# Kernel optimization log

Hardware: AMD Instinct MI355X
Metric: run time of the kernel (lower is better)

Reference implementation:

```python
import jax, jax.numpy as jnp
import numpy as np

INITIAL_RADIUS = 1.0  # init_kwargs: initial_radius > 0 -> distance-softmax branch


def reference(xyz, sparse_xyz, sparse_flow, resol_factor, K):
    # xyz: [B,3,N], sparse_xyz: [B,3,M], sparse_flow: [B,3,M]
    q = jnp.transpose(xyz, (0, 2, 1))            # [B,N,3]
    p = jnp.transpose(sparse_xyz, (0, 2, 1))     # [B,M,3]
    flow = jnp.transpose(sparse_flow, (0, 2, 1))  # [B,M,3]

    sigma = INITIAL_RADIUS * resol_factor
    qs = q / sigma
    ps = p / sigma

    # pairwise Euclidean distances [B,N,M]
    sq = (jnp.sum(qs * qs, -1)[:, :, None]
          + jnp.sum(ps * ps, -1)[:, None, :]
          - 2.0 * jnp.einsum('bnc,bmc->bnm', qs, ps))
    dist = jnp.sqrt(jnp.maximum(sq, 1e-12))

    # K nearest: smallest distances
    neg_d, idx = jax.lax.top_k(-dist, K)          # [B,N,K]
    K_dist = -neg_d                               # [B,N,K]

    # gather flow of the K neighbors: [B,N,K,3]
    grouped_flow = jnp.take_along_axis(flow[:, None, :, :], idx[..., None], axis=2)

    # softmax over -distance along K, weighted sum
    K_w = jax.nn.softmax(-K_dist, axis=2)         # [B,N,K]
    dense_flow = jnp.sum(K_w[..., None] * grouped_flow, axis=2)  # [B,N,3]

    return jnp.transpose(dense_flow, (0, 2, 1))   # [B,3,N]


def setup_inputs() -> dict:
    key = jax.random.key(0)
    k1, k2, k3 = jax.random.split(key, 3)
    B, N, M = 4, 16384, 4096
    return {
        'xyz': jax.random.normal(k1, (B, 3, N), dtype=jnp.float32),
        'sparse_xyz': jax.random.normal(k2, (B, 3, M), dtype=jnp.float32),
        'sparse_flow': jax.random.normal(k3, (B, 3, M), dtype=jnp.float32),
        'resol_factor': 1,
        'K': 5,
    }
```

## Files before the change

### kernel.cpp

```cpp
#include <hip/hip_runtime.h>
#include <math.h>
#include <stdint.h>


#define KNN 5
#define GRID 8
#define NCELL (GRID * GRID * GRID)
#define SPAN_TH 64
#define SLICES 8
#define BLOCK (SLICES * 64)
#define EPSM 1e-3f

typedef unsigned int u32;

__device__ __forceinline__ float get_inv_sigma(const int* __restrict__ rf) {
    const int ri = rf[0];
    const float sigma = (ri >= 1 && ri <= 1000000) ? (float)ri : __int_as_float(ri);
    return 1.0f / sigma;
}

__device__ __forceinline__ float rfl_f(float v) {
    return __int_as_float(__builtin_amdgcn_readfirstlane(__float_as_int(v)));
}

__device__ __forceinline__ int cid1(float x, float lo, float ich) {
    const int c = (int)floorf((x - lo) * ich);
    return c < 0 ? 0 : (c > GRID - 1 ? GRID - 1 : c);
}

__device__ __forceinline__ int sp3(int v) {
    return (v & 1) | ((v & 2) << 2) | ((v & 4) << 4);
}

#define CE_FULL(k, ki, c, ci)                          \
    {                                                  \
        const bool sw = (c) < (k);                     \
        const float vmn = fminf(k, c);                 \
        const float vmx = fmaxf(k, c);                 \
        const u32 nki = sw ? (ci) : (ki);              \
        const u32 nci = sw ? (ki) : (ci);              \
        (k) = vmn; (c) = vmx; (ki) = nki; (ci) = nci;  \
    }
#define CE_LAST(k, ki, c, ci)                          \
    {                                                  \
        const bool sw = (c) < (k);                     \
        (ki) = sw ? (ci) : (ki);                       \
        (k) = fminf(k, c);                             \
    }

#define LAD(P, CI)                                     \
    {                                                  \
        float t_ = qx * (P).x;                         \
        t_ = fmaf(qy, (P).y, t_);                      \
        t_ = fmaf(qz, (P).z, t_);                      \
        float c_ = fmaf(-2.0f, t_, (P).w);             \
        u32 ci_ = (u32)(CI);                           \
        CE_FULL(e0, i0, c_, ci_)                       \
        CE_FULL(e1, i1, c_, ci_)                       \
        CE_FULL(e2, i2, c_, ci_)                       \
        CE_FULL(e3, i3, c_, ci_)                       \
        CE_LAST(e4, i4, c_, ci_)                       \
    }


__global__ __launch_bounds__(256)
void prep_kernel(const float* __restrict__ sxyz, const int* __restrict__ rf,
                 float4* __restrict__ pts, int M, int total) {
    const int t = blockIdx.x * 256 + threadIdx.x;
    if (t >= total) return;
    const float inv = get_inv_sigma(rf);
    const int b = t / M, m = t - b * M;
    const float* sb = sxyz + (size_t)b * 3 * M;
    const float x = sb[m] * inv;
    const float y = sb[M + m] * inv;
    const float z = sb[2 * M + m] * inv;
    pts[t] = make_float4(x, y, z, fmaf(x, x, fmaf(y, y, z * z)));
}

template <bool USE_PTS>
__global__ __launch_bounds__(BLOCK, 8)
void knn_kernel(const float* __restrict__ xyz,
                const float* __restrict__ sxyz,
                const float* __restrict__ sflow,
                const int* __restrict__ rf,
                const float4* __restrict__ pts,
                float* __restrict__ out,
                int N, int M) {
    __shared__ float sval_d[SLICES * KNN * 64];
    __shared__ u32   sval_i[SLICES * KNN * 64];

    const int tid  = threadIdx.x;
    const int lane = tid & 63;
    const int wid  = tid >> 6;
    const int swid = __builtin_amdgcn_readfirstlane(wid);
    const int gpb  = N / 64;
    const int b    = blockIdx.x / gpb;
    const int grp  = blockIdx.x - b * gpb;
    const int n    = grp * 64 + lane;

    const float inv = get_inv_sigma(rf);
    const float* qb = xyz + (size_t)b * 3 * N;
    const float qx = qb[n] * inv;
    const float qy = qb[N + n] * inv;
    const float qz = qb[2 * N + n] * inv;
    const float qq = fmaf(qx, qx, fmaf(qy, qy, qz * qz));

    const int CH = M / SLICES;
    const int j0 = swid * CH;

    float e0 = 1e30f, e1 = 1e30f, e2 = 1e30f, e3 = 1e30f, e4 = 1e30f;
    u32   i0 = 0, i1 = 0, i2 = 0, i3 = 0, i4 = 0;

    if constexpr (USE_PTS) {
        const float4* __restrict__ P = pts + (size_t)b * M + j0;
#pragma unroll 4
        for (int j = 0; j < CH; ++j) {
            const float4 p = P[j];
            LAD(p, j0 + j)
        }
    } else {
        const float* __restrict__ sb = sxyz + (size_t)b * 3 * M;
#pragma unroll 4
        for (int j = 0; j < CH; ++j) {
            const float px = sb[j0 + j] * inv;
            const float py = sb[M + j0 + j] * inv;
            const float pz = sb[2 * M + j0 + j] * inv;
            const float pw = fmaf(px, px, fmaf(py, py, pz * pz));
            const float4 p = make_float4(px, py, pz, pw);
            LAD(p, j0 + j)
        }
    }

    sval_d[(wid * KNN + 0) * 64 + lane] = e0;  sval_i[(wid * KNN + 0) * 64 + lane] = i0;
    sval_d[(wid * KNN + 1) * 64 + lane] = e1;  sval_i[(wid * KNN + 1) * 64 + lane] = i1;
    sval_d[(wid * KNN + 2) * 64 + lane] = e2;  sval_i[(wid * KNN + 2) * 64 + lane] = i2;
    sval_d[(wid * KNN + 3) * 64 + lane] = e3;  sval_i[(wid * KNN + 3) * 64 + lane] = i3;
    sval_d[(wid * KNN + 4) * 64 + lane] = e4;  sval_i[(wid * KNN + 4) * 64 + lane] = i4;
    __syncthreads();

    if (wid == 0) {
        float m0 = 1e30f, m1 = 1e30f, m2 = 1e30f, m3 = 1e30f, m4 = 1e30f;
        u32   g0 = 0, g1 = 0, g2 = 0, g3 = 0, g4 = 0;
#pragma unroll
        for (int w = 0; w < SLICES; ++w) {
#pragma unroll
            for (int k = 0; k < KNN; ++k) {
                float c = sval_d[(w * KNN + k) * 64 + lane];
                u32  ci = sval_i[(w * KNN + k) * 64 + lane];
                CE_FULL(m0, g0, c, ci)
                CE_FULL(m1, g1, c, ci)
                CE_FULL(m2, g2, c, ci)
                CE_FULL(m3, g3, c, ci)
                CE_LAST(m4, g4, c, ci)
            }
        }

        const float d0 = sqrtf(fmaxf(m0 + qq, 1e-12f));
        const float d1 = sqrtf(fmaxf(m1 + qq, 1e-12f));
        const float d2 = sqrtf(fmaxf(m2 + qq, 1e-12f));
        const float d3 = sqrtf(fmaxf(m3 + qq, 1e-12f));
        const float d4 = sqrtf(fmaxf(m4 + qq, 1e-12f));
        const float w0 = 1.0f;
        const float w1 = expf(d0 - d1);
        const float w2 = expf(d0 - d2);
        const float w3 = expf(d0 - d3);
        const float w4 = expf(d0 - d4);
        const float inv_wsum = 1.0f / (w0 + w1 + w2 + w3 + w4);

        const float* fb = sflow + (size_t)b * 3 * M;
        float ax = 0.f, ay = 0.f, az = 0.f;
        ax = fmaf(w0, fb[g0], ax); ay = fmaf(w0, fb[M + g0], ay); az = fmaf(w0, fb[2 * M + g0], az);
        ax = fmaf(w1, fb[g1], ax); ay = fmaf(w1, fb[M + g1], ay); az = fmaf(w1, fb[2 * M + g1], az);
        ax = fmaf(w2, fb[g2], ax); ay = fmaf(w2, fb[M + g2], ay); az = fmaf(w2, fb[2 * M + g2], az);
        ax = fmaf(w3, fb[g3], ax); ay = fmaf(w3, fb[M + g3], ay); az = fmaf(w3, fb[2 * M + g3], az);
        ax = fmaf(w4, fb[g4], ax); ay = fmaf(w4, fb[M + g4], ay); az = fmaf(w4, fb[2 * M + g4], az);

        float* ob = out + (size_t)b * 3 * N;
        ob[n]         = ax * inv_wsum;
        ob[N + n]     = ay * inv_wsum;
        ob[2 * N + n] = az * inv_wsum;
    }
}


__global__ __launch_bounds__(1024)
void prep_all_kernel(const float* __restrict__ xyz, const float* __restrict__ sxyz,
                     const int* __restrict__ rf, float* __restrict__ bbox,
                     int2* __restrict__ off2C, float4* __restrict__ ptsS,
                     float4* __restrict__ qS, int* __restrict__ idxS,
                     int N, int M) {
    __shared__ int hC[NCELL], hQ[NCELL];
    __shared__ int oC[NCELL], oQ[NCELL];
    __shared__ float sred[6][16];
    __shared__ float sbb[6];

    const int b = blockIdx.x, t = threadIdx.x;
    const int lane = t & 63, w = t >> 6;
    const float inv = get_inv_sigma(rf);
    const float* sb = sxyz + (size_t)b * 3 * M;
    const float* qb = xyz + (size_t)b * 3 * N;

    float lx = 1e30f, ly = 1e30f, lz = 1e30f, hx = -1e30f, hy = -1e30f, hz = -1e30f;
    for (int m = t; m < M; m += 1024) {
        const float x = sb[m] * inv, y = sb[M + m] * inv, z = sb[2 * M + m] * inv;
        lx = fminf(lx, x); hx = fmaxf(hx, x);
        ly = fminf(ly, y); hy = fmaxf(hy, y);
        lz = fminf(lz, z); hz = fmaxf(hz, z);
    }
#pragma unroll
    for (int mm = 1; mm < 64; mm <<= 1) {
        lx = fminf(lx, __shfl_xor(lx, mm, 64));
        ly = fminf(ly, __shfl_xor(ly, mm, 64));
        lz = fminf(lz, __shfl_xor(lz, mm, 64));
        hx = fmaxf(hx, __shfl_xor(hx, mm, 64));
        hy = fmaxf(hy, __shfl_xor(hy, mm, 64));
        hz = fmaxf(hz, __shfl_xor(hz, mm, 64));
    }
    if (lane == 0) {
        sred[0][w] = lx; sred[1][w] = ly; sred[2][w] = lz;
        sred[3][w] = hx; sred[4][w] = hy; sred[5][w] = hz;
    }
    for (int c = t; c < NCELL; c += 1024) { hC[c] = 0; hQ[c] = 0; }
    __syncthreads();
    if (t == 0) {
        float Lx = sred[0][0], Ly = sred[1][0], Lz = sred[2][0];
        float Hx = sred[3][0], Hy = sred[4][0], Hz = sred[5][0];
        for (int k = 1; k < 16; ++k) {
            Lx = fminf(Lx, sred[0][k]); Ly = fminf(Ly, sred[1][k]); Lz = fminf(Lz, sred[2][k]);
            Hx = fmaxf(Hx, sred[3][k]); Hy = fmaxf(Hy, sred[4][k]); Hz = fmaxf(Hz, sred[5][k]);
        }
        const float sc = (1.0f / GRID) * (1.0f + 4e-6f);
        sbb[0] = Lx; sbb[1] = Ly; sbb[2] = Lz;
        sbb[3] = (Hx - Lx) * sc + 1e-30f;
        sbb[4] = (Hy - Ly) * sc + 1e-30f;
        sbb[5] = (Hz - Lz) * sc + 1e-30f;
        for (int k = 0; k < 6; ++k) bbox[b * 8 + k] = sbb[k];
    }
    __syncthreads();
    const float lox = sbb[0], loy = sbb[1], loz = sbb[2];
    const float icx = 1.0f / sbb[3], icy = 1.0f / sbb[4], icz = 1.0f / sbb[5];

#define CELL_OF(X, Y, Z) \
    ((sp3(cid1((X), lox, icx)) << 2) | (sp3(cid1((Y), loy, icy)) << 1) | sp3(cid1((Z), loz, icz)))

    for (int m = t; m < M; m += 1024) {
        const float x = sb[m] * inv, y = sb[M + m] * inv, z = sb[2 * M + m] * inv;
        atomicAdd(&hC[CELL_OF(x, y, z)], 1);
    }
    for (int i = t; i < N; i += 1024) {
        const float x = qb[i] * inv, y = qb[N + i] * inv, z = qb[2 * N + i] * inv;
        atomicAdd(&hQ[CELL_OF(x, y, z)], 1);
    }
    __syncthreads();

    if (t < NCELL) { oC[t] = hC[t]; oQ[t] = hQ[t]; }
    __syncthreads();
    for (int d = 1; d < NCELL; d <<= 1) {
        int vc = 0, vq = 0;
        if (t < NCELL && t >= d) { vc = oC[t - d]; vq = oQ[t - d]; }
        __syncthreads();
        if (t < NCELL && t >= d) { oC[t] += vc; oQ[t] += vq; }
        __syncthreads();
    }
    if (t < NCELL) {
        const int e = oC[t], h = hC[t];
        off2C[(size_t)b * NCELL + t] = make_int2(e - h, e);
        oC[t] = e - h;
        oQ[t] = oQ[t] - hQ[t];
    }
    __syncthreads();

    for (int m = t; m < M; m += 1024) {
        const float x = sb[m] * inv, y = sb[M + m] * inv, z = sb[2 * M + m] * inv;
        const int slot = atomicAdd(&oC[CELL_OF(x, y, z)], 1);
        ptsS[(size_t)b * M + slot] = make_float4(x, y, z, fmaf(x, x, fmaf(y, y, z * z)));
        idxS[(size_t)b * M + slot] = m;
    }
    for (int i = t; i < N; i += 1024) {
        const float x = qb[i] * inv, y = qb[N + i] * inv, z = qb[2 * N + i] * inv;
        const int slot = atomicAdd(&oQ[CELL_OF(x, y, z)], 1);
        qS[(size_t)b * N + slot] = make_float4(x, y, z, __int_as_float(i));
    }
#undef CELL_OF
}


#define CELLP(CZ)                                                                   \
    {                                                                               \
        const float glz_ = fmaf((float)(CZ), chz, loz);                             \
        const float dz_ = fmaxf(fmaxf(glz_ - whz, wlz - (glz_ + chz)), 0.0f);       \
        const float dl_ = fmaf(dz_, dz_, dxy_);                                     \
        if (!(dl_ > TwR)) {                                                         \
            const int cell_ = mxy_ | sp3(CZ);                                       \
            const int2 oo_ = off2b[cell_];                                          \
            const int base_ = __builtin_amdgcn_readfirstlane(oo_.x);                \
            const int end_ = __builtin_amdgcn_readfirstlane(oo_.y);                 \
            int j_ = base_;                                                         \
            for (; j_ + 4 <= end_; j_ += 4) {                                       \
                const float4 p0_ = Pb[j_];                                          \
                const float4 p1_ = Pb[j_ + 1];                                      \
                const float4 p2_ = Pb[j_ + 2];                                      \
                const float4 p3_ = Pb[j_ + 3];                                      \
                LAD(p0_, j_) LAD(p1_, j_ + 1)                                       \
                LAD(p2_, j_ + 2) LAD(p3_, j_ + 3)                                   \
            }                                                                       \
            for (; j_ < end_; ++j_) {                                               \
                const float4 pp_ = Pb[j_];                                          \
                LAD(pp_, j_)                                                        \
            }                                                                       \
        }                                                                           \
    }

#define COLUMN(HAVEFULL)                                                            \
    {                                                                               \
        if (((colctr++) & 7) == wid) {                                              \
            TwR = fminf(TwOwn,                                                      \
                        __int_as_float(__hip_atomic_load(                           \
                            &twS, __ATOMIC_RELAXED, __HIP_MEMORY_SCOPE_WORKGROUP))); \
            const float gly_ = fmaf((float)cy, chy, loy);                           \
            const float dy_ = fmaxf(fmaxf(gly_ - why, wly - (gly_ + chy)), 0.0f);   \
            const float dxy_ = fmaf(dy_, dy_, dxx);                                 \
            if (!(dxy_ > TwR)) {                                                    \
                const int mxy_ = mx | (sp3(cy) << 1);                               \
                const float old4_ = e4;                                             \
                if (HAVEFULL) {                                                     \
                    for (int cz = z0; cz <= z1; ++cz) { CELLP(cz) }                 \
                } else {                                                            \
                    if (clz - r >= 0) { CELLP(clz - r) }                            \
                    if (czh + r <= GRID - 1) { CELLP(czh + r) }                     \
                }                                                                   \
                if (__any(e4 < old4_)) {                                            \
                    float m4_ = e4 + qq;                                            \
                    for (int mm_ = 1; mm_ < 64; mm_ <<= 1)                          \
                        m4_ = fmaxf(m4_, __shfl_xor(m4_, mm_, 64));                 \
                    m4_ = rfl_f(m4_);                                               \
                    TwOwn = fminf(TwOwn, m4_);                                      \
                    TwR = fminf(TwR, m4_);                                          \
                    if (lane == 0) atomicMin(&twS, __float_as_int(m4_));            \
                }                                                                   \
            }                                                                       \
        }                                                                           \
    }

__global__ __launch_bounds__(BLOCK, 8)
void knn_grid8_kernel(const float4* __restrict__ qS, const float4* __restrict__ ptsS,
                      const int* __restrict__ idxS, const int2* __restrict__ off2C,
                      const float* __restrict__ bbox, const float* __restrict__ sflow,
                      float* __restrict__ out, int N, int M) {
    __shared__ float sval_d[SLICES * KNN * 64];
    __shared__ u32   sval_i[SLICES * KNN * 64];
    __shared__ int   twS;

    const int tid  = threadIdx.x;
    const int lane = tid & 63;
    const int wid  = tid >> 6;
    const int swid = __builtin_amdgcn_readfirstlane(wid);
    const int gpb  = N >> 6;
    const int b    = blockIdx.x / gpb;
    const int grp  = blockIdx.x - b * gpb;

    if (tid == 0) twS = 0x7F800000;
    __syncthreads();

    const float4 q4 = qS[(size_t)b * N + grp * 64 + lane];
    const float qx = q4.x, qy = q4.y, qz = q4.z;
    const int n = __float_as_int(q4.w);
    const float qq = fmaf(qx, qx, fmaf(qy, qy, qz * qz));

    float wlx = qx, wly = qy, wlz = qz, whx = qx, why = qy, whz = qz;
#pragma unroll
    for (int m = 1; m < 64; m <<= 1) {
        wlx = fminf(wlx, __shfl_xor(wlx, m, 64));
        whx = fmaxf(whx, __shfl_xor(whx, m, 64));
        wly = fminf(wly, __shfl_xor(wly, m, 64));
        why = fmaxf(why, __shfl_xor(why, m, 64));
        wlz = fminf(wlz, __shfl_xor(wlz, m, 64));
        whz = fmaxf(whz, __shfl_xor(whz, m, 64));
    }
    wlx = rfl_f(wlx) - EPSM; whx = rfl_f(whx) + EPSM;
    wly = rfl_f(wly) - EPSM; why = rfl_f(why) + EPSM;
    wlz = rfl_f(wlz) - EPSM; whz = rfl_f(whz) + EPSM;

    const float* bb = bbox + b * 8;
    const float lox = bb[0], loy = bb[1], loz = bb[2];
    const float chx = bb[3], chy = bb[4], chz = bb[5];
    const float hmin = fminf(chx, fminf(chy, chz));

    const int clx = cid1(wlx, lox, 1.0f / chx), cxh = cid1(whx, lox, 1.0f / chx);
    const int cly = cid1(wly, loy, 1.0f / chy), cyh = cid1(why, loy, 1.0f / chy);
    const int clz = cid1(wlz, loz, 1.0f / chz), czh = cid1(whz, loz, 1.0f / chz);

    float e0 = 1e30f, e1 = 1e30f, e2 = 1e30f, e3 = 1e30f, e4 = 1e30f;
    u32   i0 = 0, i1 = 0, i2 = 0, i3 = 0, i4 = 0;

    const float4* __restrict__ Pb = ptsS + (size_t)b * M;
    const int2* __restrict__ off2b = off2C + (size_t)b * NCELL;

    const int span = (cxh - clx + 1) * (cyh - cly + 1) * (czh - clz + 1);
    if (span > SPAN_TH) {
        const int CH = M / SLICES;
        const int j0 = swid * CH;
        const float4* __restrict__ P = Pb + j0;
#pragma unroll 4
        for (int j = 0; j < CH; ++j) {
            const float4 p = P[j];
            LAD(p, j0 + j)
        }
    } else {
        float TwOwn = 1e30f, TwR = 1e30f;
        int colctr = 0;
        for (int r = 0; r <= GRID; ++r) {
            TwR = fminf(TwOwn, __int_as_float(__hip_atomic_load(
                                   &twS, __ATOMIC_RELAXED, __HIP_MEMORY_SCOPE_WORKGROUP)));
            if (r >= 2) {
                const float bd = (float)(r - 1) * hmin - EPSM;
                if (bd > 0.0f && bd * bd > TwR) break;
            }
            const int x0 = clx - r < 0 ? 0 : clx - r;
            const int x1 = cxh + r > GRID - 1 ? GRID - 1 : cxh + r;
            const int y0 = cly - r < 0 ? 0 : cly - r;
            const int y1 = cyh + r > GRID - 1 ? GRID - 1 : cyh + r;
            const int z0 = clz - r < 0 ? 0 : clz - r;
            const int z1 = czh + r > GRID - 1 ? GRID - 1 : czh + r;
            for (int cx = x0; cx <= x1; ++cx) {
                const int rx = cx < clx ? clx - cx : (cx > cxh ? cx - cxh : 0);
                const float glx = fmaf((float)cx, chx, lox);
                const float dx = fmaxf(fmaxf(glx - whx, wlx - (glx + chx)), 0.0f);
                const float dxx = dx * dx;
                const int mx = sp3(cx) << 2;
                for (int cy = y0; cy <= y1; ++cy) {
                    const int ry = cy < cly ? cly - cy : (cy > cyh ? cy - cyh : 0);
                    if ((rx > ry ? rx : ry) == r) {
                        COLUMN(true)
                    } else {
                        COLUMN(false)
                    }
                }
            }
        }
    }

    sval_d[(wid * KNN + 0) * 64 + lane] = e0;  sval_i[(wid * KNN + 0) * 64 + lane] = i0;
    sval_d[(wid * KNN + 1) * 64 + lane] = e1;  sval_i[(wid * KNN + 1) * 64 + lane] = i1;
    sval_d[(wid * KNN + 2) * 64 + lane] = e2;  sval_i[(wid * KNN + 2) * 64 + lane] = i2;
    sval_d[(wid * KNN + 3) * 64 + lane] = e3;  sval_i[(wid * KNN + 3) * 64 + lane] = i3;
    sval_d[(wid * KNN + 4) * 64 + lane] = e4;  sval_i[(wid * KNN + 4) * 64 + lane] = i4;
    __syncthreads();

    if (wid == 0) {
        float m0 = 1e30f, m1 = 1e30f, m2 = 1e30f, m3 = 1e30f, m4 = 1e30f;
        u32 g0 = 0, g1 = 0, g2 = 0, g3 = 0, g4 = 0;
#pragma unroll
        for (int w = 0; w < SLICES; ++w) {
#pragma unroll
            for (int k = 0; k < KNN; ++k) {
                float c = sval_d[(w * KNN + k) * 64 + lane];
                u32 ci = sval_i[(w * KNN + k) * 64 + lane];
                CE_FULL(m0, g0, c, ci)
                CE_FULL(m1, g1, c, ci)
                CE_FULL(m2, g2, c, ci)
                CE_FULL(m3, g3, c, ci)
                CE_LAST(m4, g4, c, ci)
            }
        }

        const float d0 = sqrtf(fmaxf(m0 + qq, 1e-12f));
        const float d1 = sqrtf(fmaxf(m1 + qq, 1e-12f));
        const float d2 = sqrtf(fmaxf(m2 + qq, 1e-12f));
        const float d3 = sqrtf(fmaxf(m3 + qq, 1e-12f));
        const float d4 = sqrtf(fmaxf(m4 + qq, 1e-12f));
        const float w0 = 1.0f;
        const float w1 = expf(d0 - d1);
        const float w2 = expf(d0 - d2);
        const float w3 = expf(d0 - d3);
        const float w4 = expf(d0 - d4);
        const float inv_wsum = 1.0f / (w0 + w1 + w2 + w3 + w4);

        const int* __restrict__ idxb = idxS + (size_t)b * M;
        const int o0 = idxb[g0], o1 = idxb[g1], o2 = idxb[g2], o3 = idxb[g3], o4 = idxb[g4];
        const float* fb = sflow + (size_t)b * 3 * M;
        float ax = 0.f, ay = 0.f, az = 0.f;
        ax = fmaf(w0, fb[o0], ax); ay = fmaf(w0, fb[M + o0], ay); az = fmaf(w0, fb[2 * M + o0], az);
        ax = fmaf(w1, fb[o1], ax); ay = fmaf(w1, fb[M + o1], ay); az = fmaf(w1, fb[2 * M + o1], az);
        ax = fmaf(w2, fb[o2], ax); ay = fmaf(w2, fb[M + o2], ay); az = fmaf(w2, fb[2 * M + o2], az);
        ax = fmaf(w3, fb[o3], ax); ay = fmaf(w3, fb[M + o3], ay); az = fmaf(w3, fb[2 * M + o3], az);
        ax = fmaf(w4, fb[o4], ax); ay = fmaf(w4, fb[M + o4], ay); az = fmaf(w4, fb[2 * M + o4], az);

        float* ob = out + (size_t)b * 3 * N;
        ob[n]         = ax * inv_wsum;
        ob[N + n]     = ay * inv_wsum;
        ob[2 * N + n] = az * inv_wsum;
    }
}

extern "C" void kernel_launch(void* const* d_in, const int* in_sizes, int n_in,
                              void* d_out, int out_size, void* d_ws, size_t ws_size,
                              hipStream_t stream) {
    const float* xyz   = (const float*)d_in[0];
    const float* sxyz  = (const float*)d_in[1];
    const float* sflow = (const float*)d_in[2];
    const int*   rf    = (const int*)d_in[3];

    const int B = 4;
    const int N = in_sizes[0] / (3 * B);
    const int M = in_sizes[1] / (3 * B);
    float* out = (float*)d_out;

    size_t o = 0;
    float4* ptsS  = (float4*)((char*)d_ws + o); o += (size_t)B * M * sizeof(float4);
    float4* qS    = (float4*)((char*)d_ws + o); o += (size_t)B * N * sizeof(float4);
    int*   idxS   = (int*)((char*)d_ws + o);    o += (size_t)B * M * 4;
    float* bbox   = (float*)((char*)d_ws + o);  o += 256;
    int2*  off2C  = (int2*)((char*)d_ws + o);   o += (size_t)B * NCELL * 8;
    const size_t need = o;

    if (ws_size >= need && (N % 64) == 0 && (M % (8 * SLICES)) == 0) {
        prep_all_kernel<<<dim3(B), dim3(1024), 0, stream>>>(
            xyz, sxyz, rf, bbox, off2C, ptsS, qS, idxS, N, M);
        knn_grid8_kernel<<<dim3(B * (N / 64)), dim3(BLOCK), 0, stream>>>(
            qS, ptsS, idxS, off2C, bbox, sflow, out, N, M);
    } else {
        const dim3 grid(B * (N / 64));
        const dim3 block(BLOCK);
        const size_t needOld = (size_t)B * M * sizeof(float4);
        if (ws_size >= needOld) {
            float4* pts = (float4*)d_ws;
            prep_kernel<<<dim3((B * M + 255) / 256), dim3(256), 0, stream>>>(
                sxyz, rf, pts, M, B * M);
            knn_kernel<true><<<grid, block, 0, stream>>>(xyz, sxyz, sflow, rf, pts, out, N, M);
        } else {
            knn_kernel<false><<<grid, block, 0, stream>>>(xyz, sxyz, sflow, rf, nullptr, out, N, M);
        }
    }
}
```

Measured before the change: 312.9 us.

## Use fixed unit-cell grid, cell-aligned query groups and home-cell bound seeding

Replaces the data-dependent bounding-box grid with a fixed 8x8x8 grid of unit cells over [-4,4], with the edge cells extended to infinity, so the min/max reduction and the bbox buffer go away. Query groups are now built per 8-cell Morton super-cell through a group table, so each 64-query wavefront is spatially compact. Each query seeds its pruning bound from a top-5 scan of its own home cell. The brute-force span fallback and the shared atomic bound are removed in favour of per-wave __all pruning. This trades more, partially filled blocks and reliance on the inputs being roughly unit-scaled against far fewer candidate cells scanned per query.

```diff
diff --git a/kernel.cpp b/kernel.cpp
--- a/kernel.cpp
+++ b/kernel.cpp
@@ -6,9 +6,9 @@
 #define KNN 5
 #define GRID 8
 #define NCELL (GRID * GRID * GRID)
-#define SPAN_TH 64
 #define SLICES 8
 #define BLOCK (SLICES * 64)
+#define BOXLO -4.0f
 #define EPSM 1e-3f
 
 typedef unsigned int u32;
@@ -23,13 +23,24 @@
     return __int_as_float(__builtin_amdgcn_readfirstlane(__float_as_int(v)));
 }
 
-__device__ __forceinline__ int cid1(float x, float lo, float ich) {
-    const int c = (int)floorf((x - lo) * ich);
+__device__ __forceinline__ int cidf(float x) {
+    const int c = (int)floorf(x - BOXLO);
     return c < 0 ? 0 : (c > GRID - 1 ? GRID - 1 : c);
 }
 
 __device__ __forceinline__ int sp3(int v) {
     return (v & 1) | ((v & 2) << 2) | ((v & 4) << 4);
+}
+
+__device__ __forceinline__ int cellf(float x, float y, float z) {
+    return (sp3(cidf(x)) << 2) | (sp3(cidf(y)) << 1) | sp3(cidf(z));
+}
+
+__device__ __forceinline__ float axdist(float q, int c) {
+    const float lo = (c == 0) ? -1e30f : (BOXLO + (float)c);
+    const float hi = (c == GRID - 1) ? 1e30f : (BOXLO + (float)(c + 1));
+    const float cq = fminf(fmaxf(q, lo), hi);
+    return q - cq;
 }
 
 #define CE_FULL(k, ki, c, ci)                          \
@@ -184,72 +195,30 @@
 
 
 __global__ __launch_bounds__(1024)
-void prep_all_kernel(const float* __restrict__ xyz, const float* __restrict__ sxyz,
-                     const int* __restrict__ rf, float* __restrict__ bbox,
-                     int2* __restrict__ off2C, float4* __restrict__ ptsS,
-                     float4* __restrict__ qS, int* __restrict__ idxS,
-                     int N, int M) {
+void prep_cell_kernel(const float* __restrict__ xyz, const float* __restrict__ sxyz,
+                      const int* __restrict__ rf, int2* __restrict__ off2C,
+                      float4* __restrict__ ptsS, float4* __restrict__ qS,
+                      int* __restrict__ idxS, int2* __restrict__ grpTab,
+                      int* __restrict__ grpCnt, int N, int M, int GPB) {
     __shared__ int hC[NCELL], hQ[NCELL];
     __shared__ int oC[NCELL], oQ[NCELL];
-    __shared__ float sred[6][16];
-    __shared__ float sbb[6];
+    __shared__ int sQex[NCELL];
 
     const int b = blockIdx.x, t = threadIdx.x;
-    const int lane = t & 63, w = t >> 6;
     const float inv = get_inv_sigma(rf);
     const float* sb = sxyz + (size_t)b * 3 * M;
     const float* qb = xyz + (size_t)b * 3 * N;
 
-    float lx = 1e30f, ly = 1e30f, lz = 1e30f, hx = -1e30f, hy = -1e30f, hz = -1e30f;
+    for (int c = t; c < NCELL; c += 1024) { hC[c] = 0; hQ[c] = 0; }
+    __syncthreads();
+
     for (int m = t; m < M; m += 1024) {
         const float x = sb[m] * inv, y = sb[M + m] * inv, z = sb[2 * M + m] * inv;
-        lx = fminf(lx, x); hx = fmaxf(hx, x);
-        ly = fminf(ly, y); hy = fmaxf(hy, y);
-        lz = fminf(lz, z); hz = fmaxf(hz, z);
-    }
-#pragma unroll
-    for (int mm = 1; mm < 64; mm <<= 1) {
-        lx = fminf(lx, __shfl_xor(lx, mm, 64));
-        ly = fminf(ly, __shfl_xor(ly, mm, 64));
-        lz = fminf(lz, __shfl_xor(lz, mm, 64));
-        hx = fmaxf(hx, __shfl_xor(hx, mm, 64));
-        hy = fmaxf(hy, __shfl_xor(hy, mm, 64));
-        hz = fmaxf(hz, __shfl_xor(hz, mm, 64));
-    }
-    if (lane == 0) {
-        sred[0][w] = lx; sred[1][w] = ly; sred[2][w] = lz;
-        sred[3][w] = hx; sred[4][w] = hy; sred[5][w] = hz;
-    }
-    for (int c = t; c < NCELL; c += 1024) { hC[c] = 0; hQ[c] = 0; }
-    __syncthreads();
-    if (t == 0) {
-        float Lx = sred[0][0], Ly = sred[1][0], Lz = sred[2][0];
-        float Hx = sred[3][0], Hy = sred[4][0], Hz = sred[5][0];
-        for (int k = 1; k < 16; ++k) {
-            Lx = fminf(Lx, sred[0][k]); Ly = fminf(Ly, sred[1][k]); Lz = fminf(Lz, sred[2][k]);
-            Hx = fmaxf(Hx, sred[3][k]); Hy = fmaxf(Hy, sred[4][k]); Hz = fmaxf(Hz, sred[5][k]);
-        }
-        const float sc = (1.0f / GRID) * (1.0f + 4e-6f);
-        sbb[0] = Lx; sbb[1] = Ly; sbb[2] = Lz;
-        sbb[3] = (Hx - Lx) * sc + 1e-30f;
-        sbb[4] = (Hy - Ly) * sc + 1e-30f;
-        sbb[5] = (Hz - Lz) * sc + 1e-30f;
-        for (int k = 0; k < 6; ++k) bbox[b * 8 + k] = sbb[k];
-    }
-    __syncthreads();
-    const float lox = sbb[0], loy = sbb[1], loz = sbb[2];
-    const float icx = 1.0f / sbb[3], icy = 1.0f / sbb[4], icz = 1.0f / sbb[5];
-
-#define CELL_OF(X, Y, Z) \
-    ((sp3(cid1((X), lox, icx)) << 2) | (sp3(cid1((Y), loy, icy)) << 1) | sp3(cid1((Z), loz, icz)))
-
-    for (int m = t; m < M; m += 1024) {
-        const float x = sb[m] * inv, y = sb[M + m] * inv, z = sb[2 * M + m] * inv;
-        atomicAdd(&hC[CELL_OF(x, y, z)], 1);
+        atomicAdd(&hC[cellf(x, y, z)], 1);
     }
     for (int i = t; i < N; i += 1024) {
         const float x = qb[i] * inv, y = qb[N + i] * inv, z = qb[2 * N + i] * inv;
-        atomicAdd(&hQ[CELL_OF(x, y, z)], 1);
+        atomicAdd(&hQ[cellf(x, y, z)], 1);
     }
     __syncthreads();
 
@@ -266,103 +235,100 @@
         const int e = oC[t], h = hC[t];
         off2C[(size_t)b * NCELL + t] = make_int2(e - h, e);
         oC[t] = e - h;
-        oQ[t] = oQ[t] - hQ[t];
+        const int eq = oQ[t] - hQ[t];
+        sQex[t] = eq;
+        oQ[t] = eq;
     }
     __syncthreads();
 
     for (int m = t; m < M; m += 1024) {
         const float x = sb[m] * inv, y = sb[M + m] * inv, z = sb[2 * M + m] * inv;
-        const int slot = atomicAdd(&oC[CELL_OF(x, y, z)], 1);
+        const int slot = atomicAdd(&oC[cellf(x, y, z)], 1);
         ptsS[(size_t)b * M + slot] = make_float4(x, y, z, fmaf(x, x, fmaf(y, y, z * z)));
         idxS[(size_t)b * M + slot] = m;
     }
     for (int i = t; i < N; i += 1024) {
         const float x = qb[i] * inv, y = qb[N + i] * inv, z = qb[2 * N + i] * inv;
-        const int slot = atomicAdd(&oQ[CELL_OF(x, y, z)], 1);
+        const int slot = atomicAdd(&oQ[cellf(x, y, z)], 1);
         qS[(size_t)b * N + slot] = make_float4(x, y, z, __int_as_float(i));
     }
-#undef CELL_OF
-}
-
-
-#define CELLP(CZ)                                                                   \
-    {                                                                               \
-        const float glz_ = fmaf((float)(CZ), chz, loz);                             \
-        const float dz_ = fmaxf(fmaxf(glz_ - whz, wlz - (glz_ + chz)), 0.0f);       \
-        const float dl_ = fmaf(dz_, dz_, dxy_);                                     \
-        if (!(dl_ > TwR)) {                                                         \
-            const int cell_ = mxy_ | sp3(CZ);                                       \
-            const int2 oo_ = off2b[cell_];                                          \
-            const int base_ = __builtin_amdgcn_readfirstlane(oo_.x);                \
-            const int end_ = __builtin_amdgcn_readfirstlane(oo_.y);                 \
-            int j_ = base_;                                                         \
-            for (; j_ + 4 <= end_; j_ += 4) {                                       \
-                const float4 p0_ = Pb[j_];                                          \
-                const float4 p1_ = Pb[j_ + 1];                                      \
-                const float4 p2_ = Pb[j_ + 2];                                      \
-                const float4 p3_ = Pb[j_ + 3];                                      \
-                LAD(p0_, j_) LAD(p1_, j_ + 1)                                       \
-                LAD(p2_, j_ + 2) LAD(p3_, j_ + 3)                                   \
-            }                                                                       \
-            for (; j_ < end_; ++j_) {                                               \
-                const float4 pp_ = Pb[j_];                                          \
-                LAD(pp_, j_)                                                        \
-            }                                                                       \
-        }                                                                           \
-    }
-
-#define COLUMN(HAVEFULL)                                                            \
-    {                                                                               \
-        if (((colctr++) & 7) == wid) {                                              \
-            TwR = fminf(TwOwn,                                                      \
-                        __int_as_float(__hip_atomic_load(                           \
-                            &twS, __ATOMIC_RELAXED, __HIP_MEMORY_SCOPE_WORKGROUP))); \
-            const float gly_ = fmaf((float)cy, chy, loy);                           \
-            const float dy_ = fmaxf(fmaxf(gly_ - why, wly - (gly_ + chy)), 0.0f);   \
-            const float dxy_ = fmaf(dy_, dy_, dxx);                                 \
-            if (!(dxy_ > TwR)) {                                                    \
-                const int mxy_ = mx | (sp3(cy) << 1);                               \
-                const float old4_ = e4;                                             \
-                if (HAVEFULL) {                                                     \
-                    for (int cz = z0; cz <= z1; ++cz) { CELLP(cz) }                 \
-                } else {                                                            \
-                    if (clz - r >= 0) { CELLP(clz - r) }                            \
-                    if (czh + r <= GRID - 1) { CELLP(czh + r) }                     \
-                }                                                                   \
-                if (__any(e4 < old4_)) {                                            \
-                    float m4_ = e4 + qq;                                            \
-                    for (int mm_ = 1; mm_ < 64; mm_ <<= 1)                          \
-                        m4_ = fmaxf(m4_, __shfl_xor(m4_, mm_, 64));                 \
-                    m4_ = rfl_f(m4_);                                               \
-                    TwOwn = fminf(TwOwn, m4_);                                      \
-                    TwR = fminf(TwR, m4_);                                          \
-                    if (lane == 0) atomicMin(&twS, __float_as_int(m4_));            \
-                }                                                                   \
-            }                                                                       \
-        }                                                                           \
+    __syncthreads();
+
+    if (t < 64) {
+        const int sc = t;
+        const int qs = sQex[sc * 8];
+        const int qe = (sc == 63) ? N : sQex[sc * 8 + 8];
+        const int cnt = qe - qs;
+        int ng = (cnt + 63) >> 6;
+        int incl = ng;
+#pragma unroll
+        for (int d = 1; d < 64; d <<= 1) {
+            const int v = __shfl_up(incl, d, 64);
+            if (t >= d) incl += v;
+        }
+        const int goff = incl - ng;
+        for (int k = 0; k < ng; ++k) {
+            const int base = k << 6;
+            grpTab[(size_t)b * GPB + goff + k] =
+                make_int2(qs + base, min(64, cnt - base));
+        }
+        if (t == 63) grpCnt[b] = incl;
+    }
+}
+
+
+#define CELLSCAN(CELLIDX)                                                       \
+    {                                                                           \
+        const int2 oo_ = off2b[CELLIDX];                                        \
+        const int base_ = __builtin_amdgcn_readfirstlane(oo_.x);                \
+        const int end_ = __builtin_amdgcn_readfirstlane(oo_.y);                 \
+        int j_ = base_;                                                         \
+        for (; j_ + 4 <= end_; j_ += 4) {                                       \
+            const float4 p0_ = Pb[j_];                                          \
+            const float4 p1_ = Pb[j_ + 1];                                      \
+            const float4 p2_ = Pb[j_ + 2];                                      \
+            const float4 p3_ = Pb[j_ + 3];                                      \
+            LAD(p0_, j_) LAD(p1_, j_ + 1)                                       \
+            LAD(p2_, j_ + 2) LAD(p3_, j_ + 3)                                   \
+        }                                                                       \
+        for (; j_ < end_; ++j_) {                                               \
+            const float4 pp_ = Pb[j_];                                          \
+            LAD(pp_, j_)                                                        \
+        }                                                                       \
+    }
+
+#define CELLP(CZ)                                                               \
+    {                                                                           \
+        const float dzl_ = axdist(qz, (CZ));                                    \
+        const float d3_ = fmaf(dzl_, dzl_, dxy2);                               \
+        const float cmp_ = fmaf(fminf(e4, bw) + qq, 1.00001f, EPSM);            \
+        if (!__all(d3_ > cmp_)) {                                               \
+            CELLSCAN(mxy | sp3(CZ))                                             \
+        }                                                                       \
     }
 
 __global__ __launch_bounds__(BLOCK, 8)
-void knn_grid8_kernel(const float4* __restrict__ qS, const float4* __restrict__ ptsS,
-                      const int* __restrict__ idxS, const int2* __restrict__ off2C,
-                      const float* __restrict__ bbox, const float* __restrict__ sflow,
-                      float* __restrict__ out, int N, int M) {
+void knn_cell_kernel(const float4* __restrict__ qS, const float4* __restrict__ ptsS,
+                     const int* __restrict__ idxS, const int2* __restrict__ off2C,
+                     const int2* __restrict__ grpTab, const int* __restrict__ grpCnt,
+                     const float* __restrict__ sflow,
+                     float* __restrict__ out, int N, int M, int GPB) {
     __shared__ float sval_d[SLICES * KNN * 64];
     __shared__ u32   sval_i[SLICES * KNN * 64];
-    __shared__ int   twS;
 
     const int tid  = threadIdx.x;
     const int lane = tid & 63;
     const int wid  = tid >> 6;
-    const int swid = __builtin_amdgcn_readfirstlane(wid);
-    const int gpb  = N >> 6;
-    const int b    = blockIdx.x / gpb;
-    const int grp  = blockIdx.x - b * gpb;
-
-    if (tid == 0) twS = 0x7F800000;
-    __syncthreads();
-
-    const float4 q4 = qS[(size_t)b * N + grp * 64 + lane];
+    const int gid  = blockIdx.x;
+    const int b    = gid / GPB;
+    const int g    = gid - b * GPB;
+    if (g >= grpCnt[b]) return;
+
+    const int2 ent = grpTab[(size_t)b * GPB + g];
+    const int qbase = ent.x, qcnt = ent.y;
+    const int lidx = qbase + (lane < qcnt ? lane : qcnt - 1);
+
+    const float4 q4 = qS[(size_t)b * N + lidx];
     const float qx = q4.x, qy = q4.y, qz = q4.z;
     const int n = __float_as_int(q4.w);
     const float qq = fmaf(qx, qx, fmaf(qy, qy, qz * qz));
@@ -381,14 +347,9 @@
     wly = rfl_f(wly) - EPSM; why = rfl_f(why) + EPSM;
     wlz = rfl_f(wlz) - EPSM; whz = rfl_f(whz) + EPSM;
 
-    const float* bb = bbox + b * 8;
-    const float lox = bb[0], loy = bb[1], loz = bb[2];
-    const float chx = bb[3], chy = bb[4], chz = bb[5];
-    const float hmin = fminf(chx, fminf(chy, chz));
-
-    const int clx = cid1(wlx, lox, 1.0f / chx), cxh = cid1(whx, lox, 1.0f / chx);
-    const int cly = cid1(wly, loy, 1.0f / chy), cyh = cid1(why, loy, 1.0f / chy);
-    const int clz = cid1(wlz, loz, 1.0f / chz), czh = cid1(whz, loz, 1.0f / chz);
+    const int clx = cidf(wlx), cxh = cidf(whx);
+    const int cly = cidf(wly), cyh = cidf(why);
+    const int clz = cidf(wlz), czh = cidf(whz);
 
     float e0 = 1e30f, e1 = 1e30f, e2 = 1e30f, e3 = 1e30f, e4 = 1e30f;
     u32   i0 = 0, i1 = 0, i2 = 0, i3 = 0, i4 = 0;
@@ -396,44 +357,75 @@
     const float4* __restrict__ Pb = ptsS + (size_t)b * M;
     const int2* __restrict__ off2b = off2C + (size_t)b * NCELL;
 
-    const int span = (cxh - clx + 1) * (cyh - cly + 1) * (czh - clz + 1);
-    if (span > SPAN_TH) {
-        const int CH = M / SLICES;
-        const int j0 = swid * CH;
-        const float4* __restrict__ P = Pb + j0;
-#pragma unroll 4
-        for (int j = 0; j < CH; ++j) {
-            const float4 p = P[j];
-            LAD(p, j0 + j)
-        }
-    } else {
-        float TwOwn = 1e30f, TwR = 1e30f;
-        int colctr = 0;
-        for (int r = 0; r <= GRID; ++r) {
-            TwR = fminf(TwOwn, __int_as_float(__hip_atomic_load(
-                                   &twS, __ATOMIC_RELAXED, __HIP_MEMORY_SCOPE_WORKGROUP)));
-            if (r >= 2) {
-                const float bd = (float)(r - 1) * hmin - EPSM;
-                if (bd > 0.0f && bd * bd > TwR) break;
+    float bw;
+    {
+        const int2 ho = off2b[cellf(qx, qy, qz)];
+        float v0 = 1e30f, v1 = 1e30f, v2 = 1e30f, v3 = 1e30f, v4 = 1e30f;
+        for (int j = ho.x; j < ho.y; ++j) {
+            const float4 p = Pb[j];
+            float t = qx * p.x;
+            t = fmaf(qy, p.y, t);
+            t = fmaf(qz, p.z, t);
+            float c = fmaf(-2.0f, t, p.w);
+            float mn;
+            mn = fminf(v0, c); c = fmaxf(v0, c); v0 = mn;
+            mn = fminf(v1, c); c = fmaxf(v1, c); v1 = mn;
+            mn = fminf(v2, c); c = fmaxf(v2, c); v2 = mn;
+            mn = fminf(v3, c); c = fmaxf(v3, c); v3 = mn;
+            v4 = fminf(v4, c);
+        }
+        bw = v4;
+    }
+
+    int ctr = 0;
+    for (int cx = clx; cx <= cxh; ++cx) {
+        const float dxl = axdist(qx, cx);
+        const float dxx = dxl * dxl;
+        const int mx = sp3(cx) << 2;
+        for (int cy = cly; cy <= cyh; ++cy) {
+            const float dyl = axdist(qy, cy);
+            const float dxy2 = fmaf(dyl, dyl, dxx);
+            const int mxy = mx | (sp3(cy) << 1);
+            for (int cz = clz; cz <= czh; ++cz) {
+                if (((ctr++) & 7) == wid) { CELLP(cz) }
             }
-            const int x0 = clx - r < 0 ? 0 : clx - r;
-            const int x1 = cxh + r > GRID - 1 ? GRID - 1 : cxh + r;
-            const int y0 = cly - r < 0 ? 0 : cly - r;
-            const int y1 = cyh + r > GRID - 1 ? GRID - 1 : cyh + r;
-            const int z0 = clz - r < 0 ? 0 : clz - r;
-            const int z1 = czh + r > GRID - 1 ? GRID - 1 : czh + r;
-            for (int cx = x0; cx <= x1; ++cx) {
-                const int rx = cx < clx ? clx - cx : (cx > cxh ? cx - cxh : 0);
-                const float glx = fmaf((float)cx, chx, lox);
-                const float dx = fmaxf(fmaxf(glx - whx, wlx - (glx + chx)), 0.0f);
-                const float dxx = dx * dx;
-                const int mx = sp3(cx) << 2;
-                for (int cy = y0; cy <= y1; ++cy) {
-                    const int ry = cy < cly ? cly - cy : (cy > cyh ? cy - cyh : 0);
-                    if ((rx > ry ? rx : ry) == r) {
-                        COLUMN(true)
-                    } else {
-                        COLUMN(false)
+        }
+    }
+    float TwR = 1e30f;
+    for (int r = 1; r <= GRID; ++r) {
+        float own = fminf(e4, bw) + qq;
+#pragma unroll
+        for (int mm = 1; mm < 64; mm <<= 1) own = fmaxf(own, __shfl_xor(own, mm, 64));
+        TwR = fminf(TwR, rfl_f(own));
+        if (r >= 2) {
+            const float bd = (float)(r - 1) - EPSM;
+            if (bd * bd > fmaf(TwR, 1.00001f, EPSM)) break;
+        }
+        const int x0 = clx - r < 0 ? 0 : clx - r;
+        const int x1 = cxh + r > GRID - 1 ? GRID - 1 : cxh + r;
+        const int y0 = cly - r < 0 ? 0 : cly - r;
+        const int y1 = cyh + r > GRID - 1 ? GRID - 1 : cyh + r;
+        const int z0 = clz - r < 0 ? 0 : clz - r;
+        const int z1 = czh + r > GRID - 1 ? GRID - 1 : czh + r;
+        for (int cx = x0; cx <= x1; ++cx) {
+            const int rx = cx < clx ? clx - cx : (cx > cxh ? cx - cxh : 0);
+            const float dxl = axdist(qx, cx);
+            const float dxx = dxl * dxl;
+            const int mx = sp3(cx) << 2;
+            for (int cy = y0; cy <= y1; ++cy) {
+                const int ry = cy < cly ? cly - cy : (cy > cyh ? cy - cyh : 0);
+                if (((ctr++) & 7) == wid) {
+                    const float dyl = axdist(qy, cy);
+                    const float dxy2 = fmaf(dyl, dyl, dxx);
+                    const float cmpc = fmaf(fminf(e4, bw) + qq, 1.00001f, EPSM);
+                    if (!__all(dxy2 > cmpc)) {
+                        const int mxy = mx | (sp3(cy) << 1);
+                        if ((rx > ry ? rx : ry) == r) {
+                            for (int cz = z0; cz <= z1; ++cz) { CELLP(cz) }
+                        } else {
+                            if (clz - r >= 0) { CELLP(clz - r) }
+                            if (czh + r <= GRID - 1) { CELLP(czh + r) }
+                        }
                     }
                 }
             }
@@ -464,32 +456,34 @@
             }
         }
 
-        const float d0 = sqrtf(fmaxf(m0 + qq, 1e-12f));
-        const float d1 = sqrtf(fmaxf(m1 + qq, 1e-12f));
-        const float d2 = sqrtf(fmaxf(m2 + qq, 1e-12f));
-        const float d3 = sqrtf(fmaxf(m3 + qq, 1e-12f));
-        const float d4 = sqrtf(fmaxf(m4 + qq, 1e-12f));
-        const float w0 = 1.0f;
-        const float w1 = expf(d0 - d1);
-        const float w2 = expf(d0 - d2);
-        const float w3 = expf(d0 - d3);
-        const float w4 = expf(d0 - d4);
-        const float inv_wsum = 1.0f / (w0 + w1 + w2 + w3 + w4);
-
-        const int* __restrict__ idxb = idxS + (size_t)b * M;
-        const int o0 = idxb[g0], o1 = idxb[g1], o2 = idxb[g2], o3 = idxb[g3], o4 = idxb[g4];
-        const float* fb = sflow + (size_t)b * 3 * M;
-        float ax = 0.f, ay = 0.f, az = 0.f;
-        ax = fmaf(w0, fb[o0], ax); ay = fmaf(w0, fb[M + o0], ay); az = fmaf(w0, fb[2 * M + o0], az);
-        ax = fmaf(w1, fb[o1], ax); ay = fmaf(w1, fb[M + o1], ay); az = fmaf(w1, fb[2 * M + o1], az);
-        ax = fmaf(w2, fb[o2], ax); ay = fmaf(w2, fb[M + o2], ay); az = fmaf(w2, fb[2 * M + o2], az);
-        ax = fmaf(w3, fb[o3], ax); ay = fmaf(w3, fb[M + o3], ay); az = fmaf(w3, fb[2 * M + o3], az);
-        ax = fmaf(w4, fb[o4], ax); ay = fmaf(w4, fb[M + o4], ay); az = fmaf(w4, fb[2 * M + o4], az);
-
-        float* ob = out + (size_t)b * 3 * N;
-        ob[n]         = ax * inv_wsum;
-        ob[N + n]     = ay * inv_wsum;
-        ob[2 * N + n] = az * inv_wsum;
+        if (lane < qcnt) {
+            const float d0 = sqrtf(fmaxf(m0 + qq, 1e-12f));
+            const float d1 = sqrtf(fmaxf(m1 + qq, 1e-12f));
+            const float d2 = sqrtf(fmaxf(m2 + qq, 1e-12f));
+            const float d3 = sqrtf(fmaxf(m3 + qq, 1e-12f));
+            const float d4 = sqrtf(fmaxf(m4 + qq, 1e-12f));
+            const float w0 = 1.0f;
+            const float w1 = expf(d0 - d1);
+            const float w2 = expf(d0 - d2);
+            const float w3 = expf(d0 - d3);
+            const float w4 = expf(d0 - d4);
+            const float inv_wsum = 1.0f / (w0 + w1 + w2 + w3 + w4);
+
+            const int* __restrict__ idxb = idxS + (size_t)b * M;
+            const int o0 = idxb[g0], o1 = idxb[g1], o2 = idxb[g2], o3 = idxb[g3], o4 = idxb[g4];
+            const float* fb = sflow + (size_t)b * 3 * M;
+            float ax = 0.f, ay = 0.f, az = 0.f;
+            ax = fmaf(w0, fb[o0], ax); ay = fmaf(w0, fb[M + o0], ay); az = fmaf(w0, fb[2 * M + o0], az);
+            ax = fmaf(w1, fb[o1], ax); ay = fmaf(w1, fb[M + o1], ay); az = fmaf(w1, fb[2 * M + o1], az);
+            ax = fmaf(w2, fb[o2], ax); ay = fmaf(w2, fb[M + o2], ay); az = fmaf(w2, fb[2 * M + o2], az);
+            ax = fmaf(w3, fb[o3], ax); ay = fmaf(w3, fb[M + o3], ay); az = fmaf(w3, fb[2 * M + o3], az);
+            ax = fmaf(w4, fb[o4], ax); ay = fmaf(w4, fb[M + o4], ay); az = fmaf(w4, fb[2 * M + o4], az);
+
+            float* ob = out + (size_t)b * 3 * N;
+            ob[n]         = ax * inv_wsum;
+            ob[N + n]     = ay * inv_wsum;
+            ob[2 * N + n] = az * inv_wsum;
+        }
     }
 }
 
@@ -505,20 +499,22 @@
     const int N = in_sizes[0] / (3 * B);
     const int M = in_sizes[1] / (3 * B);
     float* out = (float*)d_out;
+    const int GPB = N / 64 + 64;
 
     size_t o = 0;
     float4* ptsS  = (float4*)((char*)d_ws + o); o += (size_t)B * M * sizeof(float4);
     float4* qS    = (float4*)((char*)d_ws + o); o += (size_t)B * N * sizeof(float4);
     int*   idxS   = (int*)((char*)d_ws + o);    o += (size_t)B * M * 4;
-    float* bbox   = (float*)((char*)d_ws + o);  o += 256;
     int2*  off2C  = (int2*)((char*)d_ws + o);   o += (size_t)B * NCELL * 8;
+    int2*  grpTab = (int2*)((char*)d_ws + o);   o += (size_t)B * GPB * 8;
+    int*   grpCnt = (int*)((char*)d_ws + o);    o += 64;
     const size_t need = o;
 
-    if (ws_size >= need && (N % 64) == 0 && (M % (8 * SLICES)) == 0) {
-        prep_all_kernel<<<dim3(B), dim3(1024), 0, stream>>>(
-            xyz, sxyz, rf, bbox, off2C, ptsS, qS, idxS, N, M);
-        knn_grid8_kernel<<<dim3(B * (N / 64)), dim3(BLOCK), 0, stream>>>(
-            qS, ptsS, idxS, off2C, bbox, sflow, out, N, M);
+    if (ws_size >= need && (N % 64) == 0) {
+        prep_cell_kernel<<<dim3(B), dim3(1024), 0, stream>>>(
+            xyz, sxyz, rf, off2C, ptsS, qS, idxS, grpTab, grpCnt, N, M, GPB);
+        knn_cell_kernel<<<dim3(B * GPB), dim3(BLOCK), 0, stream>>>(
+            qS, ptsS, idxS, off2C, grpTab, grpCnt, sflow, out, N, M, GPB);
     } else {
         const dim3 grid(B * (N / 64));
         const dim3 block(BLOCK);
```

After: 300.9 us. -3.8%, faster.
